# Performance work log

Measured on AMD Instinct MI355X. Metric: run time of the kernel, lower is better.

Reference implementation:

```python
import jax, jax.numpy as jnp
import numpy as np
import math

D_MODEL = 512
DIM_K = 512
DIM_V = 512
N_HEADS = 8


def setup_inputs() -> dict:
    key = jax.random.key(0)
    ks = jax.random.split(key, 12)
    B, S = 2, 2048
    sc = 1.0 / math.sqrt(D_MODEL)
    return {
        "x": jax.random.normal(ks[0], (B, S, D_MODEL), dtype=jnp.float32),
        "y": jax.random.normal(ks[1], (B, S, D_MODEL), dtype=jnp.float32),
        # weights stored [in, out] so linear is x @ W + b
        "Wq": jax.random.normal(ks[2], (D_MODEL, DIM_K), dtype=jnp.float32) * sc,
        "bq": jnp.zeros((DIM_K,), dtype=jnp.float32),
        "Wk": jax.random.normal(ks[3], (D_MODEL, DIM_K), dtype=jnp.float32) * sc,
        "bk": jnp.zeros((DIM_K,), dtype=jnp.float32),
        "Wv": jax.random.normal(ks[4], (D_MODEL, DIM_V), dtype=jnp.float32) * sc,
        "bv": jnp.zeros((DIM_V,), dtype=jnp.float32),
        "Wo": jax.random.normal(ks[5], (DIM_V, D_MODEL), dtype=jnp.float32) * sc,
        "bo": jnp.zeros((D_MODEL,), dtype=jnp.float32),
    }


def reference(x, y, Wq, bq, Wk, bk, Wv, bv, Wo, bo):
    B, S, _ = x.shape
    H = N_HEADS
    Dh = DIM_K // H
    Dvh = DIM_V // H
    norm = 1.0 / math.sqrt(D_MODEL)  # note: original scales by 1/sqrt(d_model)

    # torch: q(x).reshape(-1, B, S, Dh) -> heads on leading dim (row-major)
    Q = (x @ Wq + bq).reshape(-1, B, S, Dh)      # [H,B,S,Dh]
    K = (y @ Wk + bk).reshape(-1, B, S, Dh)      # [H,B,S,Dh]
    V = (y @ Wv + bv).reshape(-1, B, S, Dvh)     # [H,B,S,Dvh]

    scores = jnp.einsum('hbqd,hbkd->hbqk', Q, K) * norm  # [H,B,S,S]

    # median-threshold mask: torch.median on even n returns lower middle value
    med_idx = (S - 1) // 2
    thre = jnp.sort(scores, axis=-1)[..., med_idx:med_idx + 1]  # [H,B,S,1]
    masked = scores - thre <= 0  # mask where score <= median
    scores = jnp.where(masked, -jnp.inf, scores)

    attn = jax.nn.softmax(scores, axis=-1)
    # dropout omitted (deterministic / eval mode)
    out = jnp.einsum('hbqk,hbkd->hbqd', attn, V)  # [H,B,S,Dvh]
    out = out.reshape(B, S, -1)                   # faithful row-major reshape
    return out @ Wo + bo
```

## Files before the change

kernel.cpp:

```cpp
#include <hip/hip_runtime.h>
#include <hip/hip_bf16.h>
#include <stdint.h>

#define SEQ    2048
#define DMODEL 512
#define NPANEL 16
#define NORM   0.044194173824159216f

typedef _Float16 f16;
typedef __attribute__((ext_vector_type(8))) _Float16 half8;
typedef __attribute__((ext_vector_type(2))) _Float16 half2v;
typedef __attribute__((ext_vector_type(4))) float f32x4;
typedef __attribute__((ext_vector_type(4))) unsigned int u32x4;

__device__ __forceinline__ unsigned umin2(unsigned a, unsigned b){ return a<b?a:b; }
__device__ __forceinline__ unsigned umax2(unsigned a, unsigned b){ return a>b?a:b; }

__global__ __launch_bounds__(256) void k_cvt(const float4* __restrict__ x,
                                             const float4* __restrict__ y,
                                             f16* __restrict__ xh, f16* __restrict__ xl,
                                             f16* __restrict__ yh, f16* __restrict__ yl){
  int i = blockIdx.x*256 + threadIdx.x;
  float4 a = x[i]; float4 b = y[i];
  half2v h0 = {(f16)a.x, (f16)a.y}, h1 = {(f16)a.z, (f16)a.w};
  *(half2v*)(xh + i*4)     = h0; *(half2v*)(xh + i*4 + 2) = h1;
  half2v l0 = {(f16)(a.x-(float)h0[0]), (f16)(a.y-(float)h0[1])};
  half2v l1 = {(f16)(a.z-(float)h1[0]), (f16)(a.w-(float)h1[1])};
  *(half2v*)(xl + i*4)     = l0; *(half2v*)(xl + i*4 + 2) = l1;
  half2v g0 = {(f16)b.x, (f16)b.y}, g1 = {(f16)b.z, (f16)b.w};
  *(half2v*)(yh + i*4)     = g0; *(half2v*)(yh + i*4 + 2) = g1;
  half2v m0 = {(f16)(b.x-(float)g0[0]), (f16)(b.y-(float)g0[1])};
  half2v m1 = {(f16)(b.z-(float)g1[0]), (f16)(b.w-(float)g1[1])};
  *(half2v*)(yl + i*4)     = m0; *(half2v*)(yl + i*4 + 2) = m1;
}

__global__ __launch_bounds__(256) void k_wt(const float* __restrict__ Wq, const float* __restrict__ Wk,
                                            const float* __restrict__ Wv, const float* __restrict__ Wo,
                                            f16* __restrict__ Wth, f16* __restrict__ Wtl){
  int z = blockIdx.z;
  const float* W = (z==0)?Wq:(z==1)?Wk:(z==2)?Wv:Wo;
  __shared__ float tile[64][65];
  int k0 = blockIdx.x*64, n0 = blockIdx.y*64;
  #pragma unroll
  for (int i = 0; i < 16; ++i){
    int s = threadIdx.x + i*256; int kl2 = s>>6, nl = s&63;
    tile[kl2][nl] = W[(k0+kl2)*512 + (n0+nl)];
  }
  __syncthreads();
  #pragma unroll
  for (int i = 0; i < 16; ++i){
    int s = threadIdx.x + i*256; int nl = s>>6, kl2 = s&63;
    float v = tile[kl2][nl];
    f16 h = (f16)v;
    int idx = z*262144 + (n0+nl)*512 + (k0+kl2);
    Wth[idx] = h;
    Wtl[idx] = (f16)(v - (float)h);
  }
}

template<int FINAL>
__global__ __launch_bounds__(256) void k_gemm(const f16* __restrict__ Ah0, const f16* __restrict__ Al0,
                                              const f16* __restrict__ Ah1, const f16* __restrict__ Al1,
                                              const f16* __restrict__ Wh, const f16* __restrict__ Wl,
                                              const float* __restrict__ b0, const float* __restrict__ b1,
                                              const float* __restrict__ b2,
                                              f16* __restrict__ Oq, float* __restrict__ Of){
  int z = blockIdx.z;
  const f16* A  = (z==0) ? Ah0 : Ah1;
  const f16* Alp= (z==0) ? Al0 : Al1;
  const f16* Bh = Wh + z*262144;
  const f16* Bl = Wl + z*262144;
  const float* bias = (z==0)?b0:(z==1)?b1:b2;
  const bool split = (FINAL==0) && (z<2);
  int m0 = blockIdx.x*128, n0 = blockIdx.y*128;

  __shared__ f16 Ahs[128][40], Bhs[128][40], Als[128][40], Bls[128][40];

  int t = threadIdx.x, l = t&63, w = t>>6;
  int wr = w>>1, wc = w&1;
  int lr = l&15, lk = l>>4;

  f32x4 acc[4][4];
  #pragma unroll
  for (int i=0;i<4;++i)
    #pragma unroll
    for (int j=0;j<4;++j) acc[i][j] = (f32x4){0.f,0.f,0.f,0.f};

  for (int ks = 0; ks < 16; ++ks){
    int k0 = ks*32;
    #pragma unroll
    for (int i = 0; i < 2; ++i){
      int s = t + i*256; int r = s>>2, kc = s&3;
      *(u32x4*)(&Ahs[r][kc*8]) = *(const u32x4*)(A   + (m0+r)*512 + k0 + kc*8);
      *(u32x4*)(&Bhs[r][kc*8]) = *(const u32x4*)(Bh  + (n0+r)*512 + k0 + kc*8);
      if (split){
        *(u32x4*)(&Als[r][kc*8]) = *(const u32x4*)(Alp + (m0+r)*512 + k0 + kc*8);
        *(u32x4*)(&Bls[r][kc*8]) = *(const u32x4*)(Bl  + (n0+r)*512 + k0 + kc*8);
      }
    }
    __syncthreads();
    half8 ah[4], bh2[4], al2[4], bl2[4];
    #pragma unroll
    for (int tm = 0; tm < 4; ++tm) ah[tm]  = *(const half8*)(&Ahs[wr*64 + tm*16 + lr][lk*8]);
    #pragma unroll
    for (int tn = 0; tn < 4; ++tn) bh2[tn] = *(const half8*)(&Bhs[wc*64 + tn*16 + lr][lk*8]);
    if (split){
      #pragma unroll
      for (int tm = 0; tm < 4; ++tm) al2[tm] = *(const half8*)(&Als[wr*64 + tm*16 + lr][lk*8]);
      #pragma unroll
      for (int tn = 0; tn < 4; ++tn) bl2[tn] = *(const half8*)(&Bls[wc*64 + tn*16 + lr][lk*8]);
    }
    #pragma unroll
    for (int tm = 0; tm < 4; ++tm)
      #pragma unroll
      for (int tn = 0; tn < 4; ++tn){
        acc[tm][tn] = __builtin_amdgcn_mfma_f32_16x16x32_f16(ah[tm], bh2[tn], acc[tm][tn], 0,0,0);
        if (split){
          acc[tm][tn] = __builtin_amdgcn_mfma_f32_16x16x32_f16(ah[tm], bl2[tn], acc[tm][tn], 0,0,0);
          acc[tm][tn] = __builtin_amdgcn_mfma_f32_16x16x32_f16(al2[tm], bh2[tn], acc[tm][tn], 0,0,0);
        }
      }
    __syncthreads();
  }

  #pragma unroll
  for (int tn = 0; tn < 4; ++tn){
    int n_g = n0 + wc*64 + tn*16 + lr;
    float bv = bias[n_g];
    #pragma unroll
    for (int tm = 0; tm < 4; ++tm){
      #pragma unroll
      for (int r = 0; r < 4; ++r){
        int m_g = m0 + wr*64 + tm*16 + lk*4 + r;
        float v = acc[tm][tn][r] + bv;
        size_t idx = (size_t)m_g*512 + n_g;
        if (FINAL){
          Of[idx] = v;
        } else if (z < 2){
          f16 h = (f16)v;
          Oq[(size_t)z*4194304 + idx] = h;
          Oq[(size_t)z*4194304 + 2097152 + idx] = (f16)(v - (float)h);
        } else {
          Oq[(size_t)4*2097152 + idx] = (f16)v;
        }
      }
    }
  }
}

__global__ __launch_bounds__(256) void k_vt(const unsigned short* __restrict__ V, unsigned short* __restrict__ Vt){
  int p = blockIdx.y;
  int t = threadIdx.x;
  int d = t & 63, sc = t >> 6;
  int s0b = blockIdx.x*32 + sc*8;
  const unsigned short* Vp = V + p*131072;
  unsigned short* Vtp = Vt + p*131072;
  typedef __attribute__((ext_vector_type(8))) short short8;
  short8 vv;
  #pragma unroll
  for (int j = 0; j < 8; ++j) vv[j] = (short)Vp[(s0b + j)*64 + d];
  *(short8*)(Vtp + d*2048 + s0b) = vv;
}

__global__ __launch_bounds__(512, 6) void k_score(const f16* __restrict__ Qh, const f16* __restrict__ Ql,
                                                  const f16* __restrict__ Kh, const f16* __restrict__ Kl,
                                                  float* __restrict__ S){
  int p = blockIdx.x, qt = blockIdx.y;
  int s0 = qt*16;
  const f16* Qhp = Qh + p*131072;
  const f16* Qlp = Ql + p*131072;
  const f16* Khp = Kh + p*131072;
  const f16* Klp = Kl + p*131072;
  int t = threadIdx.x, l = t&63, w = t>>6;
  int lr = l&15, lk = l>>4;

  half8 qh[2], qlo[2];
  #pragma unroll
  for (int f = 0; f < 2; ++f){
    qh[f]  = *(const half8*)(Qhp + (s0+lr)*64 + f*32 + lk*8);
    qlo[f] = *(const half8*)(Qlp + (s0+lr)*64 + f*32 + lk*8);
  }
  float* Sb = S + (size_t)(p*2048 + s0)*2048;

  #pragma unroll 2
  for (int ct = 0; ct < 16; ++ct){
    int n = w*256 + ct*16;
    const f16* kb = Khp + (n+lr)*64 + lk*8;
    const f16* lb = Klp + (n+lr)*64 + lk*8;
    half8 kh0 = *(const half8*)(kb);
    half8 kh1 = *(const half8*)(kb + 32);
    half8 kl0 = *(const half8*)(lb);
    half8 kl1 = *(const half8*)(lb + 32);
    f32x4 c1 = (f32x4){0.f,0.f,0.f,0.f};
    f32x4 c2 = (f32x4){0.f,0.f,0.f,0.f};
    f32x4 c3 = (f32x4){0.f,0.f,0.f,0.f};
    c1 = __builtin_amdgcn_mfma_f32_16x16x32_f16(qh[0],  kh0, c1, 0,0,0);
    c2 = __builtin_amdgcn_mfma_f32_16x16x32_f16(qh[0],  kl0, c2, 0,0,0);
    c3 = __builtin_amdgcn_mfma_f32_16x16x32_f16(qlo[0], kh0, c3, 0,0,0);
    c1 = __builtin_amdgcn_mfma_f32_16x16x32_f16(qh[1],  kh1, c1, 0,0,0);
    c2 = __builtin_amdgcn_mfma_f32_16x16x32_f16(qh[1],  kl1, c2, 0,0,0);
    c3 = __builtin_amdgcn_mfma_f32_16x16x32_f16(qlo[1], kh1, c3, 0,0,0);
    #pragma unroll
    for (int r = 0; r < 4; ++r){
      Sb[(size_t)(lk*4 + r)*2048 + n + lr] = c1[r] + c2[r] + c3[r];
    }
  }
}

__global__ __launch_bounds__(256, 6) void k_sel(const float* S, f16* P, float* __restrict__ rz){
  int wid = blockIdx.x*4 + (threadIdx.x>>6);
  int l = threadIdx.x & 63;
  const float* row = S + (size_t)wid*2048;
  unsigned ov[32];
  #pragma unroll
  for (int j = 0; j < 32; ++j){
    unsigned u = __float_as_uint(row[l + j*64]);
    ov[j] = ((int)u < 0) ? ~u : (u | 0x80000000u);
  }
  unsigned umn = 0xFFFFFFFFu, umx = 0u;
  #pragma unroll
  for (int j = 0; j < 32; ++j){ umn = umin2(umn, ov[j]); umx = umax2(umx, ov[j]); }
  #pragma unroll
  for (int off2 = 1; off2 < 64; off2 <<= 1){
    umn = umin2(umn, (unsigned)__shfl_xor((int)umn, off2));
    umx = umax2(umx, (unsigned)__shfl_xor((int)umx, off2));
  }
  unsigned thr;
  {
    unsigned L = umn, R = umx;
    #pragma unroll 1
    for (;;){
      if (L >= R){ thr = R; break; }
      unsigned mid = L + ((R - L) >> 1);
      int c = 0;
      #pragma unroll
      for (int j = 0; j < 32; ++j) c += (int)__popcll(__ballot(ov[j] <= mid));
      if (c == 1024){ thr = mid; break; }
      if (c > 1024) R = mid; else L = mid + 1;
    }
  }
  unsigned bmx = (umx & 0x80000000u) ? (umx & 0x7FFFFFFFu) : ~umx;
  float mx = __uint_as_float(bmx);
  float zs = 0.f;
  f16* prow = P + (size_t)wid*4096;
  #pragma unroll
  for (int j = 0; j < 32; ++j){
    unsigned a = ov[j];
    unsigned b = (a & 0x80000000u) ? (a & 0x7FFFFFFFu) : ~a;
    float v = __uint_as_float(b);
    float wgt = (a <= thr) ? 0.f : __expf((v - mx) * NORM);
    zs += wgt;
    prow[l + j*64] = (f16)wgt;
  }
  #pragma unroll
  for (int off2 = 1; off2 < 64; off2 <<= 1) zs += __shfl_xor(zs, off2);
  if (l == 0) rz[wid] = 1.f / zs;
}

__global__ __launch_bounds__(512, 8) void k_pv(const f16* __restrict__ P, const f16* __restrict__ Vt,
                                               const float* __restrict__ rz, f16* __restrict__ O){
  int p = blockIdx.x, rt = blockIdx.y;
  int t = threadIdx.x, l = t&63, w = t>>6;
  int lr = l&15, lk = l>>4;
  int wr = w>>2, oc = w&3;
  int r0 = rt*32 + wr*16;
  const f16* prow = P + (size_t)(p*2048 + r0 + lr)*4096 + lk*8;
  const f16* vb   = Vt + p*131072 + (oc*16 + lr)*2048 + lk*8;
  f32x4 o0 = (f32x4){0.f,0.f,0.f,0.f};
  f32x4 o1 = (f32x4){0.f,0.f,0.f,0.f};
  #pragma unroll 4
  for (int kc = 0; kc < 64; ++kc){
    half8 pa = *(const half8*)(prow + kc*32);
    half8 vv = *(const half8*)(vb + kc*32);
    if (kc & 1) o1 = __builtin_amdgcn_mfma_f32_16x16x32_f16(pa, vv, o1, 0,0,0);
    else        o0 = __builtin_amdgcn_mfma_f32_16x16x32_f16(pa, vv, o0, 0,0,0);
  }
  #pragma unroll
  for (int r = 0; r < 4; ++r){
    int g = r0 + lk*4 + r;
    float val = (o0[r] + o1[r]) * rz[p*2048 + g];
    O[p*131072 + g*64 + oc*16 + lr] = (f16)val;
  }
}

__global__ __launch_bounds__(512, 4) void k_attn(const f16* __restrict__ Qh, const f16* __restrict__ Ql,
                                                 const f16* __restrict__ Kh, const f16* __restrict__ Kl,
                                                 const f16* __restrict__ Vt, f16* __restrict__ O){
  extern __shared__ char scb[];
  __shared__ float rzs[16];
  __shared__ float red[1024];
  int p = blockIdx.y, qt = blockIdx.x;
  int s0 = qt*16;
  const f16* Qhp = Qh + p*131072;
  const f16* Qlp = Ql + p*131072;
  const f16* Khp = Kh + p*131072;
  const f16* Klp = Kl + p*131072;
  const f16* Vtp = Vt + p*131072;
  int t = threadIdx.x, l = t&63, w = t>>6;
  int lr = l&15, lk = l>>4;

  half8 qh[2], ql[2];
  #pragma unroll
  for (int f = 0; f < 2; ++f){
    qh[f] = *(const half8*)(Qhp + (s0+lr)*64 + f*32 + lk*8);
    ql[f] = *(const half8*)(Qlp + (s0+lr)*64 + f*32 + lk*8);
  }

  {
    int cbase = w*128;
    #pragma unroll 2
    for (int ct = 0; ct < 8; ++ct){
      int n = cbase + ct*16;
      const f16* kb  = Khp + (n+lr)*64 + lk*8;
      const f16* kb2 = Klp + (n+lr)*64 + lk*8;
      half8 kh0 = *(const half8*)(kb),  kh1 = *(const half8*)(kb + 32);
      half8 kl0 = *(const half8*)(kb2), kl1 = *(const half8*)(kb2 + 32);
      f32x4 acc = (f32x4){0.f,0.f,0.f,0.f};
      acc = __builtin_amdgcn_mfma_f32_16x16x32_f16(qh[0], kh0, acc, 0,0,0);
      acc = __builtin_amdgcn_mfma_f32_16x16x32_f16(qh[1], kh1, acc, 0,0,0);
      acc = __builtin_amdgcn_mfma_f32_16x16x32_f16(qh[0], kl0, acc, 0,0,0);
      acc = __builtin_amdgcn_mfma_f32_16x16x32_f16(qh[1], kl1, acc, 0,0,0);
      acc = __builtin_amdgcn_mfma_f32_16x16x32_f16(ql[0], kh0, acc, 0,0,0);
      acc = __builtin_amdgcn_mfma_f32_16x16x32_f16(ql[1], kh1, acc, 0,0,0);
      #pragma unroll
      for (int r = 0; r < 4; ++r){
        int row = lk*4 + r;
        *(float*)(scb + row*4096 + (((unsigned)((n + lr)*4)) ^ ((unsigned)(lk<<6)))) = acc[r];
      }
    }
  }
  __syncthreads();

  unsigned ovA0[16], ovA1[16];
  {
    int row0 = w*2;
    unsigned C = ((unsigned)((row0>>2)&3))<<6;
    const char* rb0 = scb + row0*4096;
    const char* rb1 = rb0 + 4096;
    #pragma unroll
    for (int j = 0; j < 16; ++j){
      unsigned off = (((unsigned)((l + j*64)*4)) ^ C);
      unsigned u0 = *(const unsigned*)(rb0 + off);
      unsigned u1 = *(const unsigned*)(rb1 + off);
      ovA0[j] = ((int)u0 < 0) ? ~u0 : (u0 | 0x80000000u);
      ovA1[j] = ((int)u1 < 0) ? ~u1 : (u1 | 0x80000000u);
    }
  }
  __syncthreads();

  {
    int cbase = w*128;
    #pragma unroll 2
    for (int ct = 0; ct < 8; ++ct){
      int n = cbase + ct*16;
      const f16* kb  = Khp + (1024 + n + lr)*64 + lk*8;
      const f16* kb2 = Klp + (1024 + n + lr)*64 + lk*8;
      half8 kh0 = *(const half8*)(kb),  kh1 = *(const half8*)(kb + 32);
      half8 kl0 = *(const half8*)(kb2), kl1 = *(const half8*)(kb2 + 32);
      f32x4 acc = (f32x4){0.f,0.f,0.f,0.f};
      acc = __builtin_amdgcn_mfma_f32_16x16x32_f16(qh[0], kh0, acc, 0,0,0);
      acc = __builtin_amdgcn_mfma_f32_16x16x32_f16(qh[1], kh1, acc, 0,0,0);
      acc = __builtin_amdgcn_mfma_f32_16x16x32_f16(qh[0], kl0, acc, 0,0,0);
      acc = __builtin_amdgcn_mfma_f32_16x16x32_f16(qh[1], kl1, acc, 0,0,0);
      acc = __builtin_amdgcn_mfma_f32_16x16x32_f16(ql[0], kh0, acc, 0,0,0);
      acc = __builtin_amdgcn_mfma_f32_16x16x32_f16(ql[1], kh1, acc, 0,0,0);
      #pragma unroll
      for (int r = 0; r < 4; ++r){
        int row = lk*4 + r;
        *(float*)(scb + row*4096 + (((unsigned)((n + lr)*4)) ^ ((unsigned)(lk<<6)))) = acc[r];
      }
    }
  }
  __syncthreads();

  #pragma unroll 1
  for (int rr = 0; rr < 2; ++rr){
    int row = w*2 + rr;
    const char* rb = scb + row*4096;
    unsigned C = ((unsigned)((row>>2)&3))<<6;
    unsigned o2[16];
    #pragma unroll
    for (int j = 0; j < 16; ++j){
      unsigned u = *(const unsigned*)(rb + (((unsigned)((l + j*64)*4)) ^ C));
      o2[j] = ((int)u < 0) ? ~u : (u | 0x80000000u);
    }
    unsigned umn = 0xFFFFFFFFu, umx = 0u;
    #pragma unroll
    for (int j = 0; j < 16; ++j){
      unsigned a = (rr==0) ? ovA0[j] : ovA1[j];
      umn = umin2(umn, umin2(a, o2[j]));
      umx = umax2(umax2(umx, a), o2[j]);
    }
    #pragma unroll
    for (int off2 = 1; off2 < 64; off2 <<= 1){
      umn = umin2(umn, (unsigned)__shfl_xor((int)umn, off2));
      umx = umax2(umx, (unsigned)__shfl_xor((int)umx, off2));
    }
    unsigned thr;
    {
      unsigned L = umn, R = umx;
      #pragma unroll 1
      for (;;){
        if (L >= R){ thr = R; break; }
        unsigned mid = L + ((R - L) >> 1);
        int c = 0;
        #pragma unroll
        for (int j = 0; j < 16; ++j){
          unsigned a = (rr==0) ? ovA0[j] : ovA1[j];
          c += (int)__popcll(__ballot(a <= mid));
          c += (int)__popcll(__ballot(o2[j] <= mid));
        }
        if (c == 1024){ thr = mid; break; }
        if (c > 1024) R = mid; else L = mid + 1;
      }
    }
    unsigned bmx = (umx & 0x80000000u) ? (umx & 0x7FFFFFFFu) : ~umx;
    float mx = __uint_as_float(bmx);
    float zs = 0.f;
    unsigned g = ((unsigned)(row & 7)) << 4;
    char* pb = scb + row*4096;
    #pragma unroll
    for (int j = 0; j < 32; ++j){
      unsigned a = (j < 16) ? ((rr==0) ? ovA0[j] : ovA1[j]) : o2[j-16];
      unsigned b = (a & 0x80000000u) ? (a & 0x7FFFFFFFu) : ~a;
      float v = __uint_as_float(b);
      float wgt = (a <= thr) ? 0.f : __expf((v - mx) * NORM);
      zs += wgt;
      unsigned col = (unsigned)((j & 15)*64 + l + (j >> 4)*1024);
      *(f16*)(pb + ((col*2) ^ g)) = (f16)wgt;
    }
    #pragma unroll
    for (int off2 = 1; off2 < 64; off2 <<= 1) zs += __shfl_xor(zs, off2);
    if (l == 0) rzs[row] = 1.f / zs;
  }
  __syncthreads();

  int oc = w & 3, kh2 = w >> 2;
  f32x4 oa = (f32x4){0.f,0.f,0.f,0.f};
  #pragma unroll 4
  for (int kc = 0; kc < 32; ++kc){
    int kbase = kh2*1024 + kc*32;
    half8 pa = *(const half8*)(scb + lr*4096 + (((unsigned)((kbase + lk*8)*2)) ^ (((unsigned)(lr & 7)) << 4)));
    half8 vb = *(const half8*)(Vtp + (oc*16 + lr)*2048 + kbase + lk*8);
    oa = __builtin_amdgcn_mfma_f32_16x16x32_f16(pa, vb, oa, 0,0,0);
  }
  if (kh2 == 1){
    #pragma unroll
    for (int r = 0; r < 4; ++r) red[oc*256 + (lk*4+r)*16 + lr] = oa[r];
  }
  __syncthreads();
  if (kh2 == 0){
    #pragma unroll
    for (int r = 0; r < 4; ++r){
      int row = lk*4 + r;
      float v = (oa[r] + red[oc*256 + row*16 + lr]) * rzs[row];
      O[p*131072 + (s0+row)*64 + oc*16 + lr] = (f16)v;
    }
  }
}

extern "C" void kernel_launch(void* const* d_in, const int* in_sizes, int n_in,
                              void* d_out, int out_size, void* d_ws, size_t ws_size,
                              hipStream_t stream) {
  const float* x  = (const float*)d_in[0];
  const float* y  = (const float*)d_in[1];
  const float* Wq = (const float*)d_in[2];
  const float* bq = (const float*)d_in[3];
  const float* Wk = (const float*)d_in[4];
  const float* bk = (const float*)d_in[5];
  const float* Wv = (const float*)d_in[6];
  const float* bv = (const float*)d_in[7];
  const float* Wo = (const float*)d_in[8];
  const float* bo = (const float*)d_in[9];

  f16* ws = (f16*)d_ws;
  f16* xh  = ws;
  f16* xl  = ws + 2097152;
  f16* yh  = ws + 4194304;
  f16* yl  = ws + 6291456;
  f16* Wth = ws + 8388608;
  f16* Wtl = ws + 9437184;
  f16* QKV = ws + 10485760;
  f16* Vt  = ws;
  f16* Ob  = ws + 2097152;

  const size_t S_off  = 41943040ULL;
  const size_t S_size = 268435456ULL;
  const size_t rz_off = S_off + S_size;
  const size_t NEED   = rz_off + 131072ULL;
  bool use_split = (ws_size >= NEED);

  k_cvt<<<2048, 256, 0, stream>>>((const float4*)x, (const float4*)y, xh, xl, yh, yl);
  k_wt<<<dim3(8,8,4), 256, 0, stream>>>(Wq, Wk, Wv, Wo, Wth, Wtl);
  k_gemm<0><<<dim3(32,4,3), 256, 0, stream>>>(xh, xl, yh, yl, Wth, Wtl, bq, bk, bv, QKV, nullptr);
  k_vt<<<dim3(64,16), 256, 0, stream>>>((const unsigned short*)(QKV + 4*2097152), (unsigned short*)Vt);

  if (use_split){
    float* S  = (float*)((char*)d_ws + S_off);
    float* rz = (float*)((char*)d_ws + rz_off);
    k_score<<<dim3(16,128), 512, 0, stream>>>(QKV, QKV + 2097152, QKV + 2*2097152, QKV + 3*2097152, S);
    k_sel<<<dim3(8192), 256, 0, stream>>>(S, (f16*)S, rz);
    k_pv<<<dim3(16,64), 512, 0, stream>>>((const f16*)S, Vt, rz, Ob);
  } else {
    (void)hipFuncSetAttribute(reinterpret_cast<const void*>(k_attn),
                              hipFuncAttributeMaxDynamicSharedMemorySize, 65536);
    k_attn<<<dim3(128,16), 512, 65536, stream>>>(QKV, QKV + 2097152, QKV + 2*2097152, QKV + 3*2097152, Vt, Ob);
  }

  k_gemm<1><<<dim3(32,4,1), 256, 0, stream>>>(Ob, Ob, Ob, Ob, Wth + 3*262144, Wtl, bo, bo, bo, nullptr, (float*)d_out);
}
```

Before: 287.7 us.

## Fuse median selection with PV product and chunk score buffer by panel groups

New measurement: 363.0 us. +26.2%, slower.

```diff
diff --git a/kernel.cpp b/kernel.cpp
--- a/kernel.cpp
+++ b/kernel.cpp
@@ -162,10 +162,11 @@
   *(short8*)(Vtp + d*2048 + s0b) = vv;
 }
 
-__global__ __launch_bounds__(512, 6) void k_score(const f16* __restrict__ Qh, const f16* __restrict__ Ql,
+__global__ __launch_bounds__(512, 8) void k_score(const f16* __restrict__ Qh, const f16* __restrict__ Ql,
                                                   const f16* __restrict__ Kh, const f16* __restrict__ Kl,
-                                                  float* __restrict__ S){
-  int p = blockIdx.x, qt = blockIdx.y;
+                                                  float* __restrict__ S, int pg){
+  int pl = blockIdx.x, qt = blockIdx.y;
+  int p = pg + pl;
   int s0 = qt*16;
   const f16* Qhp = Qh + p*131072;
   const f16* Qlp = Ql + p*131072;
@@ -180,7 +181,7 @@
     qh[f]  = *(const half8*)(Qhp + (s0+lr)*64 + f*32 + lk*8);
     qlo[f] = *(const half8*)(Qlp + (s0+lr)*64 + f*32 + lk*8);
   }
-  float* Sb = S + (size_t)(p*2048 + s0)*2048;
+  float* Sb = S + ((size_t)pl*2048 + s0)*2048;
 
   #pragma unroll 2
   for (int ct = 0; ct < 16; ++ct){
@@ -202,84 +203,103 @@
     c3 = __builtin_amdgcn_mfma_f32_16x16x32_f16(qlo[1], kh1, c3, 0,0,0);
     #pragma unroll
     for (int r = 0; r < 4; ++r){
-      Sb[(size_t)(lk*4 + r)*2048 + n + lr] = c1[r] + c2[r] + c3[r];
-    }
-  }
-}
-
-__global__ __launch_bounds__(256, 6) void k_sel(const float* S, f16* P, float* __restrict__ rz){
-  int wid = blockIdx.x*4 + (threadIdx.x>>6);
-  int l = threadIdx.x & 63;
-  const float* row = S + (size_t)wid*2048;
-  unsigned ov[32];
-  #pragma unroll
-  for (int j = 0; j < 32; ++j){
-    unsigned u = __float_as_uint(row[l + j*64]);
-    ov[j] = ((int)u < 0) ? ~u : (u | 0x80000000u);
-  }
-  unsigned umn = 0xFFFFFFFFu, umx = 0u;
-  #pragma unroll
-  for (int j = 0; j < 32; ++j){ umn = umin2(umn, ov[j]); umx = umax2(umx, ov[j]); }
-  #pragma unroll
-  for (int off2 = 1; off2 < 64; off2 <<= 1){
-    umn = umin2(umn, (unsigned)__shfl_xor((int)umn, off2));
-    umx = umax2(umx, (unsigned)__shfl_xor((int)umx, off2));
-  }
-  unsigned thr;
-  {
-    unsigned L = umn, R = umx;
-    #pragma unroll 1
-    for (;;){
-      if (L >= R){ thr = R; break; }
-      unsigned mid = L + ((R - L) >> 1);
-      int c = 0;
-      #pragma unroll
-      for (int j = 0; j < 32; ++j) c += (int)__popcll(__ballot(ov[j] <= mid));
-      if (c == 1024){ thr = mid; break; }
-      if (c > 1024) R = mid; else L = mid + 1;
-    }
-  }
-  unsigned bmx = (umx & 0x80000000u) ? (umx & 0x7FFFFFFFu) : ~umx;
-  float mx = __uint_as_float(bmx);
-  float zs = 0.f;
-  f16* prow = P + (size_t)wid*4096;
-  #pragma unroll
-  for (int j = 0; j < 32; ++j){
-    unsigned a = ov[j];
-    unsigned b = (a & 0x80000000u) ? (a & 0x7FFFFFFFu) : ~a;
-    float v = __uint_as_float(b);
-    float wgt = (a <= thr) ? 0.f : __expf((v - mx) * NORM);
-    zs += wgt;
-    prow[l + j*64] = (f16)wgt;
-  }
-  #pragma unroll
-  for (int off2 = 1; off2 < 64; off2 <<= 1) zs += __shfl_xor(zs, off2);
-  if (l == 0) rz[wid] = 1.f / zs;
-}
-
-__global__ __launch_bounds__(512, 8) void k_pv(const f16* __restrict__ P, const f16* __restrict__ Vt,
-                                               const float* __restrict__ rz, f16* __restrict__ O){
-  int p = blockIdx.x, rt = blockIdx.y;
+      __builtin_nontemporal_store(c1[r] + c2[r] + c3[r],
+                                  Sb + (size_t)(lk*4 + r)*2048 + n + lr);
+    }
+  }
+}
+
+__global__ __launch_bounds__(512, 8) void k_selpv(const float* __restrict__ S,
+                                                  const f16* __restrict__ Vt,
+                                                  f16* __restrict__ O, int pg){
+  extern __shared__ char scb[];
+  __shared__ float red[512];
+  __shared__ float rzs[8];
+  int pl = blockIdx.x, rt = blockIdx.y;
+  int p = pg + pl;
   int t = threadIdx.x, l = t&63, w = t>>6;
   int lr = l&15, lk = l>>4;
-  int wr = w>>2, oc = w&3;
-  int r0 = rt*32 + wr*16;
-  const f16* prow = P + (size_t)(p*2048 + r0 + lr)*4096 + lk*8;
-  const f16* vb   = Vt + p*131072 + (oc*16 + lr)*2048 + lk*8;
+
+  {
+    const float* row = S + ((size_t)pl*2048 + rt*8 + w)*2048;
+    unsigned ov[32];
+    #pragma unroll
+    for (int j = 0; j < 32; ++j){
+      unsigned u = __float_as_uint(__builtin_nontemporal_load(row + l + j*64));
+      ov[j] = ((int)u < 0) ? ~u : (u | 0x80000000u);
+    }
+    unsigned umn = 0xFFFFFFFFu, umx = 0u;
+    #pragma unroll
+    for (int j = 0; j < 32; ++j){ umn = umin2(umn, ov[j]); umx = umax2(umx, ov[j]); }
+    #pragma unroll
+    for (int off2 = 1; off2 < 64; off2 <<= 1){
+      umn = umin2(umn, (unsigned)__shfl_xor((int)umn, off2));
+      umx = umax2(umx, (unsigned)__shfl_xor((int)umx, off2));
+    }
+    unsigned thr;
+    {
+      unsigned L = umn, R = umx;
+      #pragma unroll 1
+      for (;;){
+        if (L >= R){ thr = R; break; }
+        unsigned mid = L + ((R - L) >> 1);
+        int c = 0;
+        #pragma unroll
+        for (int j = 0; j < 32; ++j) c += (int)__popcll(__ballot(ov[j] <= mid));
+        if (c == 1024){ thr = mid; break; }
+        if (c > 1024) R = mid; else L = mid + 1;
+      }
+    }
+    unsigned bmx = (umx & 0x80000000u) ? (umx & 0x7FFFFFFFu) : ~umx;
+    float mx = __uint_as_float(bmx);
+    float zs = 0.f;
+    unsigned g = ((unsigned)w) << 4;
+    char* pb = scb + w*4096;
+    #pragma unroll
+    for (int j = 0; j < 32; ++j){
+      unsigned a = ov[j];
+      unsigned b = (a & 0x80000000u) ? (a & 0x7FFFFFFFu) : ~a;
+      float v = __uint_as_float(b);
+      float wgt = (a <= thr) ? 0.f : __expf((v - mx) * NORM);
+      zs += wgt;
+      unsigned col = (unsigned)(l + j*64);
+      *(f16*)(pb + ((col*2) ^ g)) = (f16)wgt;
+    }
+    #pragma unroll
+    for (int off2 = 1; off2 < 64; off2 <<= 1) zs += __shfl_xor(zs, off2);
+    if (l == 0) rzs[w] = 1.f / zs;
+  }
+  __syncthreads();
+
+  int oc = w & 3, kh = w >> 2;
+  int qr = lr & 7;
+  const f16* vbase = Vt + (size_t)p*131072 + (oc*16 + lr)*2048 + kh*1024 + lk*8;
+  const char* pbase = scb + qr*4096;
+  unsigned pswz = ((unsigned)qr) << 4;
   f32x4 o0 = (f32x4){0.f,0.f,0.f,0.f};
   f32x4 o1 = (f32x4){0.f,0.f,0.f,0.f};
   #pragma unroll 4
-  for (int kc = 0; kc < 64; ++kc){
-    half8 pa = *(const half8*)(prow + kc*32);
-    half8 vv = *(const half8*)(vb + kc*32);
-    if (kc & 1) o1 = __builtin_amdgcn_mfma_f32_16x16x32_f16(pa, vv, o1, 0,0,0);
-    else        o0 = __builtin_amdgcn_mfma_f32_16x16x32_f16(pa, vv, o0, 0,0,0);
-  }
-  #pragma unroll
-  for (int r = 0; r < 4; ++r){
-    int g = r0 + lk*4 + r;
-    float val = (o0[r] + o1[r]) * rz[p*2048 + g];
-    O[p*131072 + g*64 + oc*16 + lr] = (f16)val;
+  for (int kc = 0; kc < 32; ++kc){
+    half8 pa = *(const half8*)(pbase + (((unsigned)((kh*1024 + kc*32 + lk*8)*2)) ^ pswz));
+    half8 vb = *(const half8*)(vbase + kc*32);
+    if (kc & 1) o1 = __builtin_amdgcn_mfma_f32_16x16x32_f16(pa, vb, o1, 0,0,0);
+    else        o0 = __builtin_amdgcn_mfma_f32_16x16x32_f16(pa, vb, o0, 0,0,0);
+  }
+  f32x4 oa;
+  #pragma unroll
+  for (int r = 0; r < 4; ++r) oa[r] = o0[r] + o1[r];
+  if (kh == 1 && lk < 2){
+    #pragma unroll
+    for (int r = 0; r < 4; ++r) red[oc*128 + (lk*4+r)*16 + lr] = oa[r];
+  }
+  __syncthreads();
+  if (kh == 0 && lk < 2){
+    #pragma unroll
+    for (int r = 0; r < 4; ++r){
+      int row = lk*4 + r;
+      float v = (oa[r] + red[oc*128 + row*16 + lr]) * rzs[row];
+      O[(size_t)p*131072 + (rt*8 + row)*64 + oc*16 + lr] = (f16)v;
+    }
   }
 }
 
@@ -484,23 +504,23 @@
   f16* Vt  = ws;
   f16* Ob  = ws + 2097152;
 
-  const size_t S_off  = 41943040ULL;
-  const size_t S_size = 268435456ULL;
-  const size_t rz_off = S_off + S_size;
-  const size_t NEED   = rz_off + 131072ULL;
-  bool use_split = (ws_size >= NEED);
+  const size_t FP16_END = 41943040ULL;
+  size_t avail = (ws_size > FP16_END) ? ws_size - FP16_END : 0;
+  int G = 0;
+  for (int g = 16; g >= 1; g >>= 1)
+    if ((size_t)g * 16777216ULL <= avail){ G = g; break; }
 
   k_cvt<<<2048, 256, 0, stream>>>((const float4*)x, (const float4*)y, xh, xl, yh, yl);
   k_wt<<<dim3(8,8,4), 256, 0, stream>>>(Wq, Wk, Wv, Wo, Wth, Wtl);
   k_gemm<0><<<dim3(32,4,3), 256, 0, stream>>>(xh, xl, yh, yl, Wth, Wtl, bq, bk, bv, QKV, nullptr);
   k_vt<<<dim3(64,16), 256, 0, stream>>>((const unsigned short*)(QKV + 4*2097152), (unsigned short*)Vt);
 
-  if (use_split){
-    float* S  = (float*)((char*)d_ws + S_off);
-    float* rz = (float*)((char*)d_ws + rz_off);
-    k_score<<<dim3(16,128), 512, 0, stream>>>(QKV, QKV + 2097152, QKV + 2*2097152, QKV + 3*2097152, S);
-    k_sel<<<dim3(8192), 256, 0, stream>>>(S, (f16*)S, rz);
-    k_pv<<<dim3(16,64), 512, 0, stream>>>((const f16*)S, Vt, rz, Ob);
+  if (G > 0){
+    float* S = (float*)((char*)d_ws + FP16_END);
+    for (int pg = 0; pg < 16; pg += G){
+      k_score<<<dim3(G,128), 512, 0, stream>>>(QKV, QKV + 2097152, QKV + 2*2097152, QKV + 3*2097152, S, pg);
+      k_selpv<<<dim3(G,256), 512, 32768, stream>>>(S, Vt, Ob, pg);
+    }
   } else {
     (void)hipFuncSetAttribute(reinterpret_cast<const void*>(k_attn),
                               hipFuncAttributeMaxDynamicSharedMemorySize, 65536);
```
